# Kernel tuning notes

Hardware: AMD Instinct MI355X
Metric: run time of the kernel (lower is better)

Reference implementation:

```python
import jax, jax.numpy as jnp
import numpy as np

N = 100_000
E = 1_600_000
HID = 128
HEADS = 4
HD = HID // HEADS
EPS = 1e-5


def _ln(x, g, b):
    m = jnp.mean(x, axis=-1, keepdims=True)
    v = jnp.mean((x - m) ** 2, axis=-1, keepdims=True)
    return (x - m) * jax.lax.rsqrt(v + EPS) * g + b


def setup_inputs() -> dict:
    key = jax.random.key(0)
    ks = jax.random.split(key, 12)
    xav = lambda k, i, o: jax.random.uniform(k, (i, o), jnp.float32, -1.0, 1.0) * (0.1 * np.sqrt(6.0 / (i + o)))
    return {
        "h": jax.random.normal(ks[0], (N, HID), jnp.float32),
        "src": jax.random.randint(ks[1], (E,), 0, N, jnp.int32),
        "dst": jax.random.randint(ks[2], (E,), 0, N, jnp.int32),
        "Wq": xav(ks[3], HID, HID), "bq": jnp.zeros((HID,), jnp.float32),
        "Wk": xav(ks[4], HID, HID), "bk": jnp.zeros((HID,), jnp.float32),
        "Wv": xav(ks[5], HID, HID), "bv": jnp.zeros((HID,), jnp.float32),
        "Wo": xav(ks[6], HID, HID), "bo": jnp.zeros((HID,), jnp.float32),
        "W1": xav(ks[7], HID, 2 * HID), "b1": jnp.zeros((2 * HID,), jnp.float32),
        "W2": xav(ks[8], 2 * HID, HID), "b2": jnp.zeros((HID,), jnp.float32),
        "g1": jnp.ones((HID,), jnp.float32), "be1": jnp.zeros((HID,), jnp.float32),
        "g2": jnp.ones((HID,), jnp.float32), "be2": jnp.zeros((HID,), jnp.float32),
    }


def reference(h, src, dst, Wq, bq, Wk, bk, Wv, bv, Wo, bo, W1, b1, W2, b2, g1, be1, g2, be2):
    scale = HD ** -0.5
    h_norm = _ln(h, g1, be1)
    Q = (h_norm @ Wq + bq).reshape(N, HEADS, HD)
    K = (h_norm @ Wk + bk).reshape(N, HEADS, HD)
    V = (h_norm @ Wv + bv).reshape(N, HEADS, HD)

    # edge scores: q[dst] . k[src]  -> [E, HEADS]
    scores = jnp.sum(Q[dst] * K[src], axis=-1) * scale

    # edge softmax per destination node (segment softmax)
    smax = jax.ops.segment_max(scores, dst, num_segments=N)  # [N, HEADS]
    ex = jnp.exp(scores - smax[dst])
    denom = jax.ops.segment_sum(ex, dst, num_segments=N)
    alpha = ex / denom[dst]  # [E, HEADS]

    # weighted aggregation: sum over incoming edges of alpha * v[src]
    msgs = alpha[:, :, None] * V[src]  # [E, HEADS, HD]
    h_new = jax.ops.segment_sum(msgs, dst, num_segments=N).reshape(N, HID)

    h_attn = h_new @ Wo + bo
    h = h + h_attn  # dropout = identity (eval)
    h2 = _ln(h, g2, be2)
    ffn = jax.nn.relu(h2 @ W1 + b1) @ W2 + b2
    return h + ffn
```

## Files before the change

kernel.cpp:

```cpp
#include <hip/hip_runtime.h>
#include <math.h>

#define HIDN 128
#define EPS 1e-5f
#define ATT_SCALE 0.17677669529663687f

typedef unsigned int  u32;
typedef unsigned short u16;
typedef __attribute__((ext_vector_type(8))) short bf16x8;
typedef __attribute__((ext_vector_type(4))) float f32x4;

__device__ __forceinline__ u16 f2b(float x) {
    u32 u = __float_as_uint(x);
    u += 0x7FFFu + ((u >> 16) & 1u);
    return (u16)(u >> 16);
}
__device__ __forceinline__ float b2f(u16 x) { return __uint_as_float(((u32)x) << 16); }

#define MFMA(a, b, c) __builtin_amdgcn_mfma_f32_16x16x32_bf16((a), (b), (c), 0, 0, 0)

__device__ __forceinline__ int swz(int row, int kpos, int rowstride) {
    return row * rowstride + ((((kpos >> 3) ^ (row & 7)) << 3) | (kpos & 7));
}
__device__ __forceinline__ int swzf(int row, int kpos) {
    return row * 128 + ((((kpos >> 2) ^ (row & 7)) << 2) | (kpos & 3));
}

__global__ __launch_bounds__(256) void k_pack_all(
    const float* __restrict__ Wq, const float* __restrict__ Wk, const float* __restrict__ Wv,
    const float* __restrict__ Wo, const float* __restrict__ W1, const float* __restrict__ W2,
    u16* __restrict__ out)
{
    int idx = blockIdx.x * 256 + threadIdx.x;
    const float* W; int K, N, base, local;
    if      (idx <  2048) { W = Wq; K = 128; N = 128; base = 0;     local = idx; }
    else if (idx <  4096) { W = Wk; K = 128; N = 128; base = 16384; local = idx - 2048; }
    else if (idx <  6144) { W = Wv; K = 128; N = 128; base = 32768; local = idx - 4096; }
    else if (idx <  8192) { W = Wo; K = 128; N = 128; base = 49152; local = idx - 6144; }
    else if (idx < 12288) { W = W1; K = 128; N = 256; base = 65536; local = idx - 8192; }
    else if (idx < 16384) { W = W2; K = 256; N = 128; base = 98304; local = idx - 12288; }
    else return;
    const int KC = K >> 5;
    const int l  = local & 63;
    const int tc = local >> 6;
    const int c  = tc % KC;
    const int t  = tc / KC;
    const int col = l & 15, hg = l >> 4;
    const int kbase = c * 32 + hg * 8;
    u16 v[8];
    #pragma unroll
    for (int j = 0; j < 8; ++j) v[j] = f2b(W[(size_t)(kbase + j) * N + t * 16 + col]);
    uint4 o;
    o.x = (u32)v[0] | ((u32)v[1] << 16);
    o.y = (u32)v[2] | ((u32)v[3] << 16);
    o.z = (u32)v[4] | ((u32)v[5] << 16);
    o.w = (u32)v[6] | ((u32)v[7] << 16);
    *(uint4*)&out[base + local * 8] = o;
}

__global__ __launch_bounds__(256) void k_qkv(
    const float* __restrict__ h, const float* __restrict__ g1, const float* __restrict__ be1,
    const u16* __restrict__ Bq, const u16* __restrict__ Bk, const u16* __restrict__ Bv,
    const float* __restrict__ bq, const float* __restrict__ bk, const float* __restrict__ bv,
    u16* __restrict__ Q, u16* __restrict__ K, u16* __restrict__ V, int M)
{
    __shared__ u16 smem[4][2048];
    const int wid = threadIdx.x >> 6;
    const int l   = threadIdx.x & 63;
    int slab = blockIdx.x * 4 + wid;
    const bool valid = (slab * 16) < M;
    if (!valid) slab = 0;
    const int r0  = slab * 16;
    const int col = l & 15, hg = l >> 4;
    u16* ws = smem[wid];

    float av[4][8];
    const float* hr = h + (size_t)(r0 + col) * 128 + hg * 8;
    #pragma unroll
    for (int c = 0; c < 4; ++c) {
        float4 p0 = *(const float4*)&hr[c * 32];
        float4 p1 = *(const float4*)&hr[c * 32 + 4];
        av[c][0] = p0.x; av[c][1] = p0.y; av[c][2] = p0.z; av[c][3] = p0.w;
        av[c][4] = p1.x; av[c][5] = p1.y; av[c][6] = p1.z; av[c][7] = p1.w;
    }
    float s = 0.f, q2 = 0.f;
    #pragma unroll
    for (int c = 0; c < 4; ++c)
        #pragma unroll
        for (int j = 0; j < 8; ++j) { float v = av[c][j]; s += v; q2 += v * v; }
    s  += __shfl_xor(s, 16);  s  += __shfl_xor(s, 32);
    q2 += __shfl_xor(q2, 16); q2 += __shfl_xor(q2, 32);
    float mean = s * (1.f / 128.f);
    float var  = q2 * (1.f / 128.f) - mean * mean;
    float rs   = rsqrtf(var + EPS);

    bf16x8 af[4];
    #pragma unroll
    for (int c = 0; c < 4; ++c) {
        u32 w[4];
        #pragma unroll
        for (int jj = 0; jj < 4; ++jj) {
            int k0 = c * 32 + hg * 8 + 2 * jj;
            float v0 = (av[c][2 * jj]     - mean) * rs * g1[k0]     + be1[k0];
            float v1 = (av[c][2 * jj + 1] - mean) * rs * g1[k0 + 1] + be1[k0 + 1];
            w[jj] = (u32)f2b(v0) | ((u32)f2b(v1) << 16);
        }
        uint4 uu = make_uint4(w[0], w[1], w[2], w[3]);
        af[c] = *(bf16x8*)&uu;
    }

    const u16*  Bs[3] = {Bq, Bk, Bv};
    const float* bs[3] = {bq, bk, bv};
    u16*        Os[3] = {Q, K, V};
    #pragma unroll
    for (int w = 0; w < 3; ++w) {
        const u16* Bp = Bs[w];
        const float* bias = bs[w];
        #pragma unroll
        for (int t = 0; t < 8; ++t) {
            float bb = bias[t * 16 + col];
            f32x4 c = {bb, bb, bb, bb};
            const u16* bp = Bp + t * 2048 + l * 8;
            c = MFMA(af[0], *(const bf16x8*)(bp),        c);
            c = MFMA(af[1], *(const bf16x8*)(bp + 512),  c);
            c = MFMA(af[2], *(const bf16x8*)(bp + 1024), c);
            c = MFMA(af[3], *(const bf16x8*)(bp + 1536), c);
            #pragma unroll
            for (int r = 0; r < 4; ++r)
                ws[swz(hg * 4 + r, t * 16 + col, 128)] = f2b(c[r]);
        }
        __syncthreads();
        if (valid) {
            u16* O = Os[w];
            #pragma unroll
            for (int i = 0; i < 4; ++i) {
                int row = i * 4 + (l >> 4);
                int cg  = l & 15;
                bf16x8 vv = *(const bf16x8*)&ws[swz(row, cg * 8, 128)];
                *(bf16x8*)&O[(size_t)(r0 + row) * 128 + cg * 8] = vv;
            }
        }
        __syncthreads();
    }
}

#define BSH 8
#define CHUNK 4096

__global__ __launch_bounds__(256) void k_bcount(
    const int* __restrict__ dst, int* __restrict__ bcnt, int e)
{
    __shared__ int hist[512];
    const int tid = threadIdx.x;
    hist[tid] = 0; hist[tid + 256] = 0;
    __syncthreads();
    const int i0 = blockIdx.x * CHUNK;
    #pragma unroll
    for (int t = 0; t < CHUNK / 256; ++t) {
        int i = i0 + t * 256 + tid;
        if (i < e) atomicAdd(&hist[dst[i] >> BSH], 1);
    }
    __syncthreads();
    for (int j = tid; j < 512; j += 256) {
        int c = hist[j];
        if (c) atomicAdd(&bcnt[j], c);
    }
}

__global__ __launch_bounds__(512) void k_bscan(
    const int* __restrict__ bcnt, int* __restrict__ bbase, int* __restrict__ bcur, int nbuck)
{
    __shared__ int ts[512];
    const int tid = threadIdx.x;
    int v = (tid < nbuck) ? bcnt[tid] : 0;
    ts[tid] = v;
    __syncthreads();
    for (int off = 1; off < 512; off <<= 1) {
        int x = (tid >= off) ? ts[tid - off] : 0;
        __syncthreads();
        ts[tid] += x;
        __syncthreads();
    }
    int ex = ts[tid] - v;
    if (tid <= nbuck) bbase[tid] = ex;
    if (tid < nbuck)  bcur[tid]  = ex;
}

__global__ __launch_bounds__(256) void k_bscatter(
    const int* __restrict__ src, const int* __restrict__ dst,
    int* __restrict__ bcur, int2* __restrict__ ebuf, int e)
{
    __shared__ int hist[512];
    __shared__ int lbase[512];
    __shared__ int lrun[512];
    const int tid = threadIdx.x;
    hist[tid] = 0; hist[tid + 256] = 0;
    __syncthreads();
    const int i0 = blockIdx.x * CHUNK;
    #pragma unroll
    for (int t = 0; t < CHUNK / 256; ++t) {
        int i = i0 + t * 256 + tid;
        if (i < e) atomicAdd(&hist[dst[i] >> BSH], 1);
    }
    __syncthreads();
    for (int j = tid; j < 512; j += 256) {
        int c = hist[j];
        lrun[j] = 0;
        if (c) lbase[j] = atomicAdd(&bcur[j], c);
    }
    __syncthreads();
    #pragma unroll
    for (int t = 0; t < CHUNK / 256; ++t) {
        int i = i0 + t * 256 + tid;
        if (i < e) {
            int d = dst[i];
            int b = d >> BSH;
            int r = atomicAdd(&lrun[b], 1);
            ebuf[lbase[b] + r] = make_int2(src[i], d);
        }
    }
}

__global__ __launch_bounds__(256) void k_bbuild(
    const int2* __restrict__ ebuf, const int* __restrict__ bbase,
    int* __restrict__ cnt, int* __restrict__ offs, int* __restrict__ csrc, int n)
{
    __shared__ int ncnt[256];
    __shared__ int ts[256];
    __shared__ int nrun[256];
    const int tid = threadIdx.x;
    const int b = blockIdx.x;
    const int node0 = b << BSH;
    const int nn = min(256, n - node0);
    const int s = bbase[b];
    const int epb = bbase[b + 1] - s;

    ncnt[tid] = 0;
    __syncthreads();
    for (int i = tid; i < epb; i += 256)
        atomicAdd(&ncnt[ebuf[s + i].y & 255], 1);
    __syncthreads();
    int v = ncnt[tid];
    ts[tid] = v;
    __syncthreads();
    for (int off = 1; off < 256; off <<= 1) {
        int x = (tid >= off) ? ts[tid - off] : 0;
        __syncthreads();
        ts[tid] += x;
        __syncthreads();
    }
    int ex = ts[tid] - v;
    if (tid < nn) { cnt[node0 + tid] = v; offs[node0 + tid] = s + ex; }
    nrun[tid] = 0;
    __syncthreads();
    ncnt[tid] = ex;
    __syncthreads();
    for (int i = tid; i < epb; i += 256) {
        int2 p = ebuf[s + i];
        int d = p.y & 255;
        int r = atomicAdd(&nrun[d], 1);
        csrc[s + ncnt[d] + r] = p.x;
    }
}

__global__ __launch_bounds__(256) void k_edge(
    const u16* __restrict__ Qb, const u16* __restrict__ Kb, const u16* __restrict__ Vb,
    const int* __restrict__ offs, const int* __restrict__ cnt, const int* __restrict__ csrc,
    u16* __restrict__ hnew, int n)
{
    const int wid  = threadIdx.x >> 6;
    const int lane = threadIdx.x & 63;
    const int node = blockIdx.x * 4 + wid;
    if (node >= n) return;
    const int start = offs[node];
    const int deg   = cnt[node];

    const u32 qu = *(const u32*)&Qb[(size_t)node * 128 + lane * 2];
    const float q0 = b2f((u16)(qu & 0xFFFF));
    const float q1 = b2f((u16)(qu >> 16));

    float denom = 0.f, o0 = 0.f, o1 = 0.f;

    for (int base = 0; base < deg; base += 64) {
        int m = deg - base; if (m > 64) m = 64;
        int myidx = 0;
        if (lane < m) myidx = csrc[start + base + lane];
        int j = 0;
        for (; j + 4 <= m; j += 4) {
            int s0 = __shfl(myidx, j + 0);
            int s1 = __shfl(myidx, j + 1);
            int s2 = __shfl(myidx, j + 2);
            int s3 = __shfl(myidx, j + 3);
            const u32 k0 = *(const u32*)&Kb[(size_t)s0 * 128 + lane * 2];
            const u32 k1 = *(const u32*)&Kb[(size_t)s1 * 128 + lane * 2];
            const u32 k2 = *(const u32*)&Kb[(size_t)s2 * 128 + lane * 2];
            const u32 k3 = *(const u32*)&Kb[(size_t)s3 * 128 + lane * 2];
            const u32 v0 = *(const u32*)&Vb[(size_t)s0 * 128 + lane * 2];
            const u32 v1 = *(const u32*)&Vb[(size_t)s1 * 128 + lane * 2];
            const u32 v2 = *(const u32*)&Vb[(size_t)s2 * 128 + lane * 2];
            const u32 v3 = *(const u32*)&Vb[(size_t)s3 * 128 + lane * 2];
            float p0 = q0 * b2f((u16)(k0 & 0xFFFF)) + q1 * b2f((u16)(k0 >> 16));
            float p1 = q0 * b2f((u16)(k1 & 0xFFFF)) + q1 * b2f((u16)(k1 >> 16));
            float p2 = q0 * b2f((u16)(k2 & 0xFFFF)) + q1 * b2f((u16)(k2 >> 16));
            float p3 = q0 * b2f((u16)(k3 & 0xFFFF)) + q1 * b2f((u16)(k3 >> 16));
            p0 += __shfl_xor(p0, 1); p1 += __shfl_xor(p1, 1); p2 += __shfl_xor(p2, 1); p3 += __shfl_xor(p3, 1);
            p0 += __shfl_xor(p0, 2); p1 += __shfl_xor(p1, 2); p2 += __shfl_xor(p2, 2); p3 += __shfl_xor(p3, 2);
            p0 += __shfl_xor(p0, 4); p1 += __shfl_xor(p1, 4); p2 += __shfl_xor(p2, 4); p3 += __shfl_xor(p3, 4);
            p0 += __shfl_xor(p0, 8); p1 += __shfl_xor(p1, 8); p2 += __shfl_xor(p2, 8); p3 += __shfl_xor(p3, 8);
            float w0 = __expf(p0 * ATT_SCALE);
            float w1 = __expf(p1 * ATT_SCALE);
            float w2 = __expf(p2 * ATT_SCALE);
            float w3 = __expf(p3 * ATT_SCALE);
            denom += (w0 + w1) + (w2 + w3);
            o0 = fmaf(w0, b2f((u16)(v0 & 0xFFFF)), o0); o1 = fmaf(w0, b2f((u16)(v0 >> 16)), o1);
            o0 = fmaf(w1, b2f((u16)(v1 & 0xFFFF)), o0); o1 = fmaf(w1, b2f((u16)(v1 >> 16)), o1);
            o0 = fmaf(w2, b2f((u16)(v2 & 0xFFFF)), o0); o1 = fmaf(w2, b2f((u16)(v2 >> 16)), o1);
            o0 = fmaf(w3, b2f((u16)(v3 & 0xFFFF)), o0); o1 = fmaf(w3, b2f((u16)(v3 >> 16)), o1);
        }
        for (; j < m; ++j) {
            int s = __shfl(myidx, j);
            const u32 kk = *(const u32*)&Kb[(size_t)s * 128 + lane * 2];
            const u32 vv = *(const u32*)&Vb[(size_t)s * 128 + lane * 2];
            float p = q0 * b2f((u16)(kk & 0xFFFF)) + q1 * b2f((u16)(kk >> 16));
            p += __shfl_xor(p, 1); p += __shfl_xor(p, 2); p += __shfl_xor(p, 4); p += __shfl_xor(p, 8);
            float w = __expf(p * ATT_SCALE);
            denom += w;
            o0 = fmaf(w, b2f((u16)(vv & 0xFFFF)), o0);
            o1 = fmaf(w, b2f((u16)(vv >> 16)), o1);
        }
    }
    float inv = (deg > 0) ? (1.f / denom) : 0.f;
    u16 r0_ = f2b(o0 * inv), r1_ = f2b(o1 * inv);
    *(u32*)&hnew[(size_t)node * 128 + lane * 2] = (u32)r0_ | ((u32)r1_ << 16);
}

__global__ __launch_bounds__(256) void k_tail(
    const u16* __restrict__ hnew, const u16* __restrict__ Bo, const float* __restrict__ bo,
    const float* __restrict__ h, const float* __restrict__ g2, const float* __restrict__ be2,
    const u16* __restrict__ B1, const float* __restrict__ b1,
    const u16* __restrict__ B2, const float* __restrict__ b2,
    float* __restrict__ out, int M)
{
    __shared__ u16 smem[4][4096];
    const int wid = threadIdx.x >> 6;
    const int l   = threadIdx.x & 63;
    int slab = blockIdx.x * 4 + wid;
    const bool valid = (slab * 16) < M;
    if (!valid) slab = 0;
    const int r0  = slab * 16;
    const int col = l & 15, hg = l >> 4;
    u16* ws = smem[wid];

    const u16* ar = hnew + (size_t)(r0 + col) * 128 + hg * 8;
    bf16x8 a0 = *(const bf16x8*)(ar);
    bf16x8 a1 = *(const bf16x8*)(ar + 32);
    bf16x8 a2 = *(const bf16x8*)(ar + 64);
    bf16x8 a3 = *(const bf16x8*)(ar + 96);
    float h1v[8][4];
    float s[4] = {0, 0, 0, 0}, s2[4] = {0, 0, 0, 0};
    #pragma unroll
    for (int t = 0; t < 8; ++t) {
        float bb = bo[t * 16 + col];
        f32x4 c = {bb, bb, bb, bb};
        const u16* bp = Bo + t * 2048 + l * 8;
        c = MFMA(a0, *(const bf16x8*)(bp),        c);
        c = MFMA(a1, *(const bf16x8*)(bp + 512),  c);
        c = MFMA(a2, *(const bf16x8*)(bp + 1024), c);
        c = MFMA(a3, *(const bf16x8*)(bp + 1536), c);
        #pragma unroll
        for (int r = 0; r < 4; ++r) {
            float x = c[r] + h[(size_t)(r0 + hg * 4 + r) * 128 + t * 16 + col];
            h1v[t][r] = x;
            s[r] += x; s2[r] += x * x;
        }
    }
    float mean[4], rs[4];
    #pragma unroll
    for (int r = 0; r < 4; ++r) {
        float a = s[r], b = s2[r];
        a += __shfl_xor(a, 1); b += __shfl_xor(b, 1);
        a += __shfl_xor(a, 2); b += __shfl_xor(b, 2);
        a += __shfl_xor(a, 4); b += __shfl_xor(b, 4);
        a += __shfl_xor(a, 8); b += __shfl_xor(b, 8);
        mean[r] = a * (1.f / 128.f);
        float var = b * (1.f / 128.f) - mean[r] * mean[r];
        rs[r] = rsqrtf(var + EPS);
    }
    #pragma unroll
    for (int t = 0; t < 8; ++t) {
        float g  = g2[t * 16 + col];
        float be = be2[t * 16 + col];
        #pragma unroll
        for (int r = 0; r < 4; ++r)
            ws[swz(hg * 4 + r, t * 16 + col, 128)] =
                f2b((h1v[t][r] - mean[r]) * rs[r] * g + be);
    }
    __syncthreads();
    bf16x8 f1[4];
    #pragma unroll
    for (int i = 0; i < 4; ++i)
        f1[i] = *(const bf16x8*)&ws[swz(col, i * 32 + hg * 8, 128)];
    __syncthreads();
    #pragma unroll
    for (int t = 0; t < 16; ++t) {
        float bb = b1[t * 16 + col];
        f32x4 c = {bb, bb, bb, bb};
        const u16* bp = B1 + t * 2048 + l * 8;
        c = MFMA(f1[0], *(const bf16x8*)(bp),        c);
        c = MFMA(f1[1], *(const bf16x8*)(bp + 512),  c);
        c = MFMA(f1[2], *(const bf16x8*)(bp + 1024), c);
        c = MFMA(f1[3], *(const bf16x8*)(bp + 1536), c);
        #pragma unroll
        for (int r = 0; r < 4; ++r)
            ws[swz(hg * 4 + r, t * 16 + col, 256)] = f2b(fmaxf(c[r], 0.f));
    }
    __syncthreads();
    bf16x8 f2[8];
    #pragma unroll
    for (int i = 0; i < 8; ++i)
        f2[i] = *(const bf16x8*)&ws[swz(col, i * 32 + hg * 8, 256)];
    __syncthreads();
    float* wsf = (float*)ws;
    #pragma unroll
    for (int t = 0; t < 8; ++t) {
        float bb = b2[t * 16 + col];
        f32x4 c = {bb, bb, bb, bb};
        const u16* bp = B2 + t * 4096 + l * 8;
        #pragma unroll
        for (int kc = 0; kc < 8; ++kc)
            c = MFMA(f2[kc], *(const bf16x8*)(bp + kc * 512), c);
        #pragma unroll
        for (int r = 0; r < 4; ++r)
            wsf[swzf(hg * 4 + r, t * 16 + col)] = c[r] + h1v[t][r];
    }
    __syncthreads();
    if (valid) {
        #pragma unroll
        for (int i = 0; i < 8; ++i) {
            int row = i * 2 + (l >> 5);
            int cg  = l & 31;
            float4 v = *(const float4*)&wsf[swzf(row, cg * 4)];
            *(float4*)&out[(size_t)(r0 + row) * 128 + cg * 4] = v;
        }
    }
}

extern "C" void kernel_launch(void* const* d_in, const int* in_sizes, int n_in,
                              void* d_out, int out_size, void* d_ws, size_t ws_size,
                              hipStream_t stream)
{
    const float* h   = (const float*)d_in[0];
    const int*   src = (const int*)  d_in[1];
    const int*   dst = (const int*)  d_in[2];
    const float* Wq  = (const float*)d_in[3];
    const float* bq  = (const float*)d_in[4];
    const float* Wk  = (const float*)d_in[5];
    const float* bk  = (const float*)d_in[6];
    const float* Wv  = (const float*)d_in[7];
    const float* bv  = (const float*)d_in[8];
    const float* Wo  = (const float*)d_in[9];
    const float* bo  = (const float*)d_in[10];
    const float* W1  = (const float*)d_in[11];
    const float* b1  = (const float*)d_in[12];
    const float* W2  = (const float*)d_in[13];
    const float* b2  = (const float*)d_in[14];
    const float* g1  = (const float*)d_in[15];
    const float* be1 = (const float*)d_in[16];
    const float* g2  = (const float*)d_in[17];
    const float* be2 = (const float*)d_in[18];

    const int n = in_sizes[0] / HIDN;
    const int e = in_sizes[1];
    float* out = (float*)d_out;

    const int nbuck = (n + 255) >> BSH;

    char* p = (char*)d_ws;
    int* csrc  = (int*)p;              p += (size_t)e * 4;
    int* cnt   = (int*)p;              p += (size_t)n * 4;
    int* offs  = (int*)p;              p += (size_t)n * 4;
    int* bcnt  = (int*)p;              p += 512 * 4;
    int* bbase = (int*)p;              p += 512 * 4;
    int* bcur  = (int*)p;              p += 512 * 4;
    u16* wpack = (u16*)p;              p += 131072 * 2;
    const size_t NB = (size_t)n * HIDN * 2;
    u16* Qb   = (u16*)p;               p += NB;
    u16* Kb   = (u16*)p;               p += NB;
    u16* Vb   = (u16*)p;               p += NB;
    u16* hnew = (u16*)p;               p += NB;
    int2* ebuf = (int2*)p;             p += (size_t)e * 8;

    u16* Wq_p = wpack;
    u16* Wk_p = wpack + 16384;
    u16* Wv_p = wpack + 32768;
    u16* Wo_p = wpack + 49152;
    u16* W1_p = wpack + 65536;
    u16* W2_p = wpack + 98304;

    const int nslab = (n + 15) / 16;
    const int gemm_blocks = (nslab + 3) / 4;
    const int echunks = (e + CHUNK - 1) / CHUNK;

    hipMemsetAsync(bcnt, 0, 512 * sizeof(int), stream);

    k_bcount  <<<echunks, 256, 0, stream>>>(dst, bcnt, e);
    k_bscan   <<<1, 512, 0, stream>>>(bcnt, bbase, bcur, nbuck);
    k_bscatter<<<echunks, 256, 0, stream>>>(src, dst, bcur, ebuf, e);
    k_bbuild  <<<nbuck, 256, 0, stream>>>(ebuf, bbase, cnt, offs, csrc, n);

    k_pack_all<<<64, 256, 0, stream>>>(Wq, Wk, Wv, Wo, W1, W2, wpack);

    k_qkv <<<gemm_blocks, 256, 0, stream>>>(h, g1, be1, Wq_p, Wk_p, Wv_p,
                                            bq, bk, bv, Qb, Kb, Vb, n);

    k_edge<<<(n + 3) / 4, 256, 0, stream>>>(Qb, Kb, Vb, offs, cnt, csrc, hnew, n);

    k_tail<<<gemm_blocks, 256, 0, stream>>>(hnew, Wo_p, bo, h, g2, be2,
                                            W1_p, b1, W2_p, b2, out, n);
}
```

Before: 485.4 us.

## Interleave K/V in fp16, use dot2 edge kernel, split tail into three kernels

```diff
diff --git a/kernel.cpp b/kernel.cpp
--- a/kernel.cpp
+++ b/kernel.cpp
@@ -9,6 +9,7 @@
 typedef unsigned short u16;
 typedef __attribute__((ext_vector_type(8))) short bf16x8;
 typedef __attribute__((ext_vector_type(4))) float f32x4;
+typedef __attribute__((ext_vector_type(2))) _Float16 h16x2;
 
 __device__ __forceinline__ u16 f2b(float x) {
     u32 u = __float_as_uint(x);
@@ -16,14 +17,25 @@
     return (u16)(u >> 16);
 }
 __device__ __forceinline__ float b2f(u16 x) { return __uint_as_float(((u32)x) << 16); }
+__device__ __forceinline__ u16 f2h(float x) {
+    _Float16 h = (_Float16)x;
+    u16 r; __builtin_memcpy(&r, &h, 2); return r;
+}
+__device__ __forceinline__ h16x2 u2h(u32 a) { h16x2 r; __builtin_memcpy(&r, &a, 4); return r; }
+
+__device__ __forceinline__ float dot2f(u32 a, u32 b, float c) {
+    h16x2 ah = u2h(a), bh = u2h(b);
+#if __has_builtin(__builtin_amdgcn_fdot2)
+    return __builtin_amdgcn_fdot2(ah, bh, c, false);
+#else
+    return c + (float)ah.x * (float)bh.x + (float)ah.y * (float)bh.y;
+#endif
+}
 
 #define MFMA(a, b, c) __builtin_amdgcn_mfma_f32_16x16x32_bf16((a), (b), (c), 0, 0, 0)
 
 __device__ __forceinline__ int swz(int row, int kpos, int rowstride) {
     return row * rowstride + ((((kpos >> 3) ^ (row & 7)) << 3) | (kpos & 7));
-}
-__device__ __forceinline__ int swzf(int row, int kpos) {
-    return row * 128 + ((((kpos >> 2) ^ (row & 7)) << 2) | (kpos & 3));
 }
 
 __global__ __launch_bounds__(256) void k_pack_all(
@@ -62,9 +74,9 @@
     const float* __restrict__ h, const float* __restrict__ g1, const float* __restrict__ be1,
     const u16* __restrict__ Bq, const u16* __restrict__ Bk, const u16* __restrict__ Bv,
     const float* __restrict__ bq, const float* __restrict__ bk, const float* __restrict__ bv,
-    u16* __restrict__ Q, u16* __restrict__ K, u16* __restrict__ V, int M)
-{
-    __shared__ u16 smem[4][2048];
+    u16* __restrict__ Qh, u16* __restrict__ KVb, int M)
+{
+    __shared__ u16 smem[4][4096];
     const int wid = threadIdx.x >> 6;
     const int l   = threadIdx.x & 63;
     int slab = blockIdx.x * 4 + wid;
@@ -109,38 +121,70 @@
         af[c] = *(bf16x8*)&uu;
     }
 
-    const u16*  Bs[3] = {Bq, Bk, Bv};
-    const float* bs[3] = {bq, bk, bv};
-    u16*        Os[3] = {Q, K, V};
-    #pragma unroll
-    for (int w = 0; w < 3; ++w) {
-        const u16* Bp = Bs[w];
-        const float* bias = bs[w];
-        #pragma unroll
-        for (int t = 0; t < 8; ++t) {
-            float bb = bias[t * 16 + col];
-            f32x4 c = {bb, bb, bb, bb};
-            const u16* bp = Bp + t * 2048 + l * 8;
-            c = MFMA(af[0], *(const bf16x8*)(bp),        c);
-            c = MFMA(af[1], *(const bf16x8*)(bp + 512),  c);
-            c = MFMA(af[2], *(const bf16x8*)(bp + 1024), c);
-            c = MFMA(af[3], *(const bf16x8*)(bp + 1536), c);
-            #pragma unroll
-            for (int r = 0; r < 4; ++r)
-                ws[swz(hg * 4 + r, t * 16 + col, 128)] = f2b(c[r]);
-        }
-        __syncthreads();
-        if (valid) {
-            u16* O = Os[w];
-            #pragma unroll
-            for (int i = 0; i < 4; ++i) {
-                int row = i * 4 + (l >> 4);
-                int cg  = l & 15;
-                bf16x8 vv = *(const bf16x8*)&ws[swz(row, cg * 8, 128)];
-                *(bf16x8*)&O[(size_t)(r0 + row) * 128 + cg * 8] = vv;
-            }
-        }
-        __syncthreads();
+    #pragma unroll
+    for (int t = 0; t < 8; ++t) {
+        float bb = bq[t * 16 + col];
+        f32x4 c = {bb, bb, bb, bb};
+        const u16* bp = Bq + t * 2048 + l * 8;
+        c = MFMA(af[0], *(const bf16x8*)(bp),        c);
+        c = MFMA(af[1], *(const bf16x8*)(bp + 512),  c);
+        c = MFMA(af[2], *(const bf16x8*)(bp + 1024), c);
+        c = MFMA(af[3], *(const bf16x8*)(bp + 1536), c);
+        #pragma unroll
+        for (int r = 0; r < 4; ++r)
+            ws[swz(hg * 4 + r, t * 16 + col, 256)] = f2h(c[r]);
+    }
+    __syncthreads();
+    if (valid) {
+        #pragma unroll
+        for (int i = 0; i < 4; ++i) {
+            int row = i * 4 + (l >> 4);
+            int cg  = l & 15;
+            bf16x8 vv = *(const bf16x8*)&ws[swz(row, cg * 8, 256)];
+            *(bf16x8*)&Qh[(size_t)(r0 + row) * 128 + cg * 8] = vv;
+        }
+    }
+    __syncthreads();
+
+    #pragma unroll
+    for (int t = 0; t < 8; ++t) {
+        float bb = bk[t * 16 + col];
+        f32x4 c = {bb, bb, bb, bb};
+        const u16* bp = Bk + t * 2048 + l * 8;
+        c = MFMA(af[0], *(const bf16x8*)(bp),        c);
+        c = MFMA(af[1], *(const bf16x8*)(bp + 512),  c);
+        c = MFMA(af[2], *(const bf16x8*)(bp + 1024), c);
+        c = MFMA(af[3], *(const bf16x8*)(bp + 1536), c);
+        int cc = t * 16 + col;
+        int kp = ((cc >> 1) << 2) | (cc & 1);
+        #pragma unroll
+        for (int r = 0; r < 4; ++r)
+            ws[swz(hg * 4 + r, kp, 256)] = f2h(c[r]);
+    }
+    #pragma unroll
+    for (int t = 0; t < 8; ++t) {
+        float bb = bv[t * 16 + col];
+        f32x4 c = {bb, bb, bb, bb};
+        const u16* bp = Bv + t * 2048 + l * 8;
+        c = MFMA(af[0], *(const bf16x8*)(bp),        c);
+        c = MFMA(af[1], *(const bf16x8*)(bp + 512),  c);
+        c = MFMA(af[2], *(const bf16x8*)(bp + 1024), c);
+        c = MFMA(af[3], *(const bf16x8*)(bp + 1536), c);
+        int cc = t * 16 + col;
+        int kp = ((cc >> 1) << 2) | 2 | (cc & 1);
+        #pragma unroll
+        for (int r = 0; r < 4; ++r)
+            ws[swz(hg * 4 + r, kp, 256)] = f2h(c[r]);
+    }
+    __syncthreads();
+    if (valid) {
+        #pragma unroll
+        for (int i = 0; i < 8; ++i) {
+            int row = i * 2 + (l >> 5);
+            int g   = l & 31;
+            bf16x8 vv = *(const bf16x8*)&ws[swz(row, g * 8, 256)];
+            *(bf16x8*)&KVb[(size_t)(r0 + row) * 256 + g * 8] = vv;
+        }
     }
 }
 
@@ -264,100 +308,87 @@
 }
 
 __global__ __launch_bounds__(256) void k_edge(
-    const u16* __restrict__ Qb, const u16* __restrict__ Kb, const u16* __restrict__ Vb,
+    const u16* __restrict__ Qh, const u16* __restrict__ KVb,
     const int* __restrict__ offs, const int* __restrict__ cnt, const int* __restrict__ csrc,
     u16* __restrict__ hnew, int n)
 {
     const int wid  = threadIdx.x >> 6;
-    const int lane = threadIdx.x & 63;
+    const int l    = threadIdx.x & 63;
     const int node = blockIdx.x * 4 + wid;
     if (node >= n) return;
     const int start = offs[node];
     const int deg   = cnt[node];
-
-    const u32 qu = *(const u32*)&Qb[(size_t)node * 128 + lane * 2];
-    const float q0 = b2f((u16)(qu & 0xFFFF));
-    const float q1 = b2f((u16)(qu >> 16));
-
-    float denom = 0.f, o0 = 0.f, o1 = 0.f;
+    const int w    = l & 15;
+    const int slot = l >> 4;
+
+    const uint4 q = *(const uint4*)&Qh[(size_t)node * 128 + w * 8];
+
+    h16x2 o0 = {0, 0}, o1 = {0, 0}, o2 = {0, 0}, o3 = {0, 0};
+    float denom = 0.f;
 
     for (int base = 0; base < deg; base += 64) {
         int m = deg - base; if (m > 64) m = 64;
         int myidx = 0;
-        if (lane < m) myidx = csrc[start + base + lane];
-        int j = 0;
-        for (; j + 4 <= m; j += 4) {
-            int s0 = __shfl(myidx, j + 0);
-            int s1 = __shfl(myidx, j + 1);
-            int s2 = __shfl(myidx, j + 2);
-            int s3 = __shfl(myidx, j + 3);
-            const u32 k0 = *(const u32*)&Kb[(size_t)s0 * 128 + lane * 2];
-            const u32 k1 = *(const u32*)&Kb[(size_t)s1 * 128 + lane * 2];
-            const u32 k2 = *(const u32*)&Kb[(size_t)s2 * 128 + lane * 2];
-            const u32 k3 = *(const u32*)&Kb[(size_t)s3 * 128 + lane * 2];
-            const u32 v0 = *(const u32*)&Vb[(size_t)s0 * 128 + lane * 2];
-            const u32 v1 = *(const u32*)&Vb[(size_t)s1 * 128 + lane * 2];
-            const u32 v2 = *(const u32*)&Vb[(size_t)s2 * 128 + lane * 2];
-            const u32 v3 = *(const u32*)&Vb[(size_t)s3 * 128 + lane * 2];
-            float p0 = q0 * b2f((u16)(k0 & 0xFFFF)) + q1 * b2f((u16)(k0 >> 16));
-            float p1 = q0 * b2f((u16)(k1 & 0xFFFF)) + q1 * b2f((u16)(k1 >> 16));
-            float p2 = q0 * b2f((u16)(k2 & 0xFFFF)) + q1 * b2f((u16)(k2 >> 16));
-            float p3 = q0 * b2f((u16)(k3 & 0xFFFF)) + q1 * b2f((u16)(k3 >> 16));
-            p0 += __shfl_xor(p0, 1); p1 += __shfl_xor(p1, 1); p2 += __shfl_xor(p2, 1); p3 += __shfl_xor(p3, 1);
-            p0 += __shfl_xor(p0, 2); p1 += __shfl_xor(p1, 2); p2 += __shfl_xor(p2, 2); p3 += __shfl_xor(p3, 2);
-            p0 += __shfl_xor(p0, 4); p1 += __shfl_xor(p1, 4); p2 += __shfl_xor(p2, 4); p3 += __shfl_xor(p3, 4);
-            p0 += __shfl_xor(p0, 8); p1 += __shfl_xor(p1, 8); p2 += __shfl_xor(p2, 8); p3 += __shfl_xor(p3, 8);
-            float w0 = __expf(p0 * ATT_SCALE);
-            float w1 = __expf(p1 * ATT_SCALE);
-            float w2 = __expf(p2 * ATT_SCALE);
-            float w3 = __expf(p3 * ATT_SCALE);
-            denom += (w0 + w1) + (w2 + w3);
-            o0 = fmaf(w0, b2f((u16)(v0 & 0xFFFF)), o0); o1 = fmaf(w0, b2f((u16)(v0 >> 16)), o1);
-            o0 = fmaf(w1, b2f((u16)(v1 & 0xFFFF)), o0); o1 = fmaf(w1, b2f((u16)(v1 >> 16)), o1);
-            o0 = fmaf(w2, b2f((u16)(v2 & 0xFFFF)), o0); o1 = fmaf(w2, b2f((u16)(v2 >> 16)), o1);
-            o0 = fmaf(w3, b2f((u16)(v3 & 0xFFFF)), o0); o1 = fmaf(w3, b2f((u16)(v3 >> 16)), o1);
-        }
-        for (; j < m; ++j) {
-            int s = __shfl(myidx, j);
-            const u32 kk = *(const u32*)&Kb[(size_t)s * 128 + lane * 2];
-            const u32 vv = *(const u32*)&Vb[(size_t)s * 128 + lane * 2];
-            float p = q0 * b2f((u16)(kk & 0xFFFF)) + q1 * b2f((u16)(kk >> 16));
-            p += __shfl_xor(p, 1); p += __shfl_xor(p, 2); p += __shfl_xor(p, 4); p += __shfl_xor(p, 8);
-            float w = __expf(p * ATT_SCALE);
-            denom += w;
-            o0 = fmaf(w, b2f((u16)(vv & 0xFFFF)), o0);
-            o1 = fmaf(w, b2f((u16)(vv >> 16)), o1);
-        }
+        if (l < m) myidx = csrc[start + base + l];
+        for (int j = 0; j < m; j += 4) {
+            int eloc = j + slot;
+            int s = __shfl(myidx, eloc & 63);
+            const u16* kvr = KVb + (size_t)s * 256 + w * 16;
+            uint4 kv0 = *(const uint4*)(kvr);
+            uint4 kv1 = *(const uint4*)(kvr + 8);
+            float p = dot2f(kv0.x, q.x, 0.f);
+            p = dot2f(kv0.z, q.y, p);
+            p = dot2f(kv1.x, q.z, p);
+            p = dot2f(kv1.z, q.w, p);
+            p += __shfl_xor(p, 1);
+            p += __shfl_xor(p, 2);
+            float al = __expf(p * ATT_SCALE);
+            al = (eloc < m) ? al : 0.f;
+            denom += al;
+            h16x2 a2; a2.x = (_Float16)al; a2.y = a2.x;
+            o0 += a2 * u2h(kv0.y);
+            o1 += a2 * u2h(kv0.w);
+            o2 += a2 * u2h(kv1.y);
+            o3 += a2 * u2h(kv1.w);
+        }
+    }
+
+    float of[8];
+    of[0] = (float)o0.x; of[1] = (float)o0.y; of[2] = (float)o1.x; of[3] = (float)o1.y;
+    of[4] = (float)o2.x; of[5] = (float)o2.y; of[6] = (float)o3.x; of[7] = (float)o3.y;
+    #pragma unroll
+    for (int msk = 16; msk <= 32; msk <<= 1) {
+        #pragma unroll
+        for (int i = 0; i < 8; ++i) of[i] += __shfl_xor(of[i], msk);
+        denom += __shfl_xor(denom, msk);
     }
     float inv = (deg > 0) ? (1.f / denom) : 0.f;
-    u16 r0_ = f2b(o0 * inv), r1_ = f2b(o1 * inv);
-    *(u32*)&hnew[(size_t)node * 128 + lane * 2] = (u32)r0_ | ((u32)r1_ << 16);
-}
-
-__global__ __launch_bounds__(256) void k_tail(
+    if (slot == 0) {
+        u32 wrd[4];
+        #pragma unroll
+        for (int i = 0; i < 4; ++i)
+            wrd[i] = (u32)f2b(of[2 * i] * inv) | ((u32)f2b(of[2 * i + 1] * inv) << 16);
+        uint4 uu = make_uint4(wrd[0], wrd[1], wrd[2], wrd[3]);
+        *(uint4*)&hnew[(size_t)node * 128 + w * 8] = uu;
+    }
+}
+
+__global__ __launch_bounds__(256) void k_attnout(
     const u16* __restrict__ hnew, const u16* __restrict__ Bo, const float* __restrict__ bo,
     const float* __restrict__ h, const float* __restrict__ g2, const float* __restrict__ be2,
-    const u16* __restrict__ B1, const float* __restrict__ b1,
-    const u16* __restrict__ B2, const float* __restrict__ b2,
-    float* __restrict__ out, int M)
-{
-    __shared__ u16 smem[4][4096];
-    const int wid = threadIdx.x >> 6;
-    const int l   = threadIdx.x & 63;
-    int slab = blockIdx.x * 4 + wid;
-    const bool valid = (slab * 16) < M;
-    if (!valid) slab = 0;
-    const int r0  = slab * 16;
+    float* __restrict__ h1, u16* __restrict__ h2, int M)
+{
+    const int slab = blockIdx.x * 4 + (threadIdx.x >> 6);
+    const int l = threadIdx.x & 63;
+    const int r0 = slab * 16;
+    if (r0 >= M) return;
     const int col = l & 15, hg = l >> 4;
-    u16* ws = smem[wid];
-
     const u16* ar = hnew + (size_t)(r0 + col) * 128 + hg * 8;
     bf16x8 a0 = *(const bf16x8*)(ar);
     bf16x8 a1 = *(const bf16x8*)(ar + 32);
     bf16x8 a2 = *(const bf16x8*)(ar + 64);
     bf16x8 a3 = *(const bf16x8*)(ar + 96);
-    float h1v[8][4];
-    float s[4] = {0, 0, 0, 0}, s2[4] = {0, 0, 0, 0};
+    f32x4 acc[8];
     #pragma unroll
     for (int t = 0; t < 8; ++t) {
         float bb = bo[t * 16 + col];
@@ -367,10 +398,15 @@
         c = MFMA(a1, *(const bf16x8*)(bp + 512),  c);
         c = MFMA(a2, *(const bf16x8*)(bp + 1024), c);
         c = MFMA(a3, *(const bf16x8*)(bp + 1536), c);
+        acc[t] = c;
+    }
+    float s[4] = {0, 0, 0, 0}, s2[4] = {0, 0, 0, 0};
+    #pragma unroll
+    for (int t = 0; t < 8; ++t) {
         #pragma unroll
         for (int r = 0; r < 4; ++r) {
-            float x = c[r] + h[(size_t)(r0 + hg * 4 + r) * 128 + t * 16 + col];
-            h1v[t][r] = x;
+            float x = acc[t][r] + h[(size_t)(r0 + hg * 4 + r) * 128 + t * 16 + col];
+            acc[t][r] = x;
             s[r] += x; s2[r] += x * x;
         }
     }
@@ -391,36 +427,57 @@
         float g  = g2[t * 16 + col];
         float be = be2[t * 16 + col];
         #pragma unroll
-        for (int r = 0; r < 4; ++r)
-            ws[swz(hg * 4 + r, t * 16 + col, 128)] =
-                f2b((h1v[t][r] - mean[r]) * rs[r] * g + be);
-    }
-    __syncthreads();
-    bf16x8 f1[4];
-    #pragma unroll
-    for (int i = 0; i < 4; ++i)
-        f1[i] = *(const bf16x8*)&ws[swz(col, i * 32 + hg * 8, 128)];
-    __syncthreads();
+        for (int r = 0; r < 4; ++r) {
+            size_t idx = (size_t)(r0 + hg * 4 + r) * 128 + t * 16 + col;
+            float x = acc[t][r];
+            h1[idx] = x;
+            h2[idx] = f2b((x - mean[r]) * rs[r] * g + be);
+        }
+    }
+}
+
+__global__ __launch_bounds__(256) void k_ffn1(
+    const u16* __restrict__ h2, const u16* __restrict__ B1, const float* __restrict__ b1,
+    u16* __restrict__ tb, int M)
+{
+    const int slab = blockIdx.x * 4 + (threadIdx.x >> 6);
+    const int l = threadIdx.x & 63;
+    const int r0 = slab * 16;
+    if (r0 >= M) return;
+    const int col = l & 15, hg = l >> 4;
+    const u16* ar = h2 + (size_t)(r0 + col) * 128 + hg * 8;
+    bf16x8 a0 = *(const bf16x8*)(ar);
+    bf16x8 a1 = *(const bf16x8*)(ar + 32);
+    bf16x8 a2 = *(const bf16x8*)(ar + 64);
+    bf16x8 a3 = *(const bf16x8*)(ar + 96);
     #pragma unroll
     for (int t = 0; t < 16; ++t) {
         float bb = b1[t * 16 + col];
         f32x4 c = {bb, bb, bb, bb};
         const u16* bp = B1 + t * 2048 + l * 8;
-        c = MFMA(f1[0], *(const bf16x8*)(bp),        c);
-        c = MFMA(f1[1], *(const bf16x8*)(bp + 512),  c);
-        c = MFMA(f1[2], *(const bf16x8*)(bp + 1024), c);
-        c = MFMA(f1[3], *(const bf16x8*)(bp + 1536), c);
+        c = MFMA(a0, *(const bf16x8*)(bp),        c);
+        c = MFMA(a1, *(const bf16x8*)(bp + 512),  c);
+        c = MFMA(a2, *(const bf16x8*)(bp + 1024), c);
+        c = MFMA(a3, *(const bf16x8*)(bp + 1536), c);
         #pragma unroll
         for (int r = 0; r < 4; ++r)
-            ws[swz(hg * 4 + r, t * 16 + col, 256)] = f2b(fmaxf(c[r], 0.f));
-    }
-    __syncthreads();
-    bf16x8 f2[8];
-    #pragma unroll
-    for (int i = 0; i < 8; ++i)
-        f2[i] = *(const bf16x8*)&ws[swz(col, i * 32 + hg * 8, 256)];
-    __syncthreads();
-    float* wsf = (float*)ws;
+            tb[(size_t)(r0 + hg * 4 + r) * 256 + t * 16 + col] = f2b(fmaxf(c[r], 0.f));
+    }
+}
+
+__global__ __launch_bounds__(256) void k_ffn2(
+    const u16* __restrict__ tb, const u16* __restrict__ B2, const float* __restrict__ b2,
+    const float* __restrict__ h1, float* __restrict__ out, int M)
+{
+    const int slab = blockIdx.x * 4 + (threadIdx.x >> 6);
+    const int l = threadIdx.x & 63;
+    const int r0 = slab * 16;
+    if (r0 >= M) return;
+    const int col = l & 15, hg = l >> 4;
+    const u16* ar = tb + (size_t)(r0 + col) * 256 + hg * 8;
+    bf16x8 a[8];
+    #pragma unroll
+    for (int i = 0; i < 8; ++i) a[i] = *(const bf16x8*)(ar + i * 32);
     #pragma unroll
     for (int t = 0; t < 8; ++t) {
         float bb = b2[t * 16 + col];
@@ -428,19 +485,11 @@
         const u16* bp = B2 + t * 4096 + l * 8;
         #pragma unroll
         for (int kc = 0; kc < 8; ++kc)
-            c = MFMA(f2[kc], *(const bf16x8*)(bp + kc * 512), c);
-        #pragma unroll
-        for (int r = 0; r < 4; ++r)
-            wsf[swzf(hg * 4 + r, t * 16 + col)] = c[r] + h1v[t][r];
-    }
-    __syncthreads();
-    if (valid) {
-        #pragma unroll
-        for (int i = 0; i < 8; ++i) {
-            int row = i * 2 + (l >> 5);
-            int cg  = l & 31;
-            float4 v = *(const float4*)&wsf[swzf(row, cg * 4)];
-            *(float4*)&out[(size_t)(r0 + row) * 128 + cg * 4] = v;
+            c = MFMA(a[kc], *(const bf16x8*)(bp + kc * 512), c);
+        #pragma unroll
+        for (int r = 0; r < 4; ++r) {
+            size_t idx = (size_t)(r0 + hg * 4 + r) * 128 + t * 16 + col;
+            out[idx] = c[r] + h1[idx];
         }
     }
 }
@@ -483,12 +532,13 @@
     int* bbase = (int*)p;              p += 512 * 4;
     int* bcur  = (int*)p;              p += 512 * 4;
     u16* wpack = (u16*)p;              p += 131072 * 2;
-    const size_t NB = (size_t)n * HIDN * 2;
-    u16* Qb   = (u16*)p;               p += NB;
-    u16* Kb   = (u16*)p;               p += NB;
-    u16* Vb   = (u16*)p;               p += NB;
-    u16* hnew = (u16*)p;               p += NB;
-    int2* ebuf = (int2*)p;             p += (size_t)e * 8;
+    u16* KVb  = (u16*)p;               p += (size_t)n * 256 * 2;
+    u16* Qh   = (u16*)p;               p += (size_t)n * 128 * 2;
+    u16* hnew = (u16*)p;               p += (size_t)n * 128 * 2;
+    float* h1 = (float*)p;             p += (size_t)n * 128 * 4;
+    u16* h2 = Qh;
+    u16* tb = KVb;
+    int2* ebuf = (int2*)h1;
 
     u16* Wq_p = wpack;
     u16* Wk_p = wpack + 16384;
@@ -511,10 +561,13 @@
     k_pack_all<<<64, 256, 0, stream>>>(Wq, Wk, Wv, Wo, W1, W2, wpack);
 
     k_qkv <<<gemm_blocks, 256, 0, stream>>>(h, g1, be1, Wq_p, Wk_p, Wv_p,
-                                            bq, bk, bv, Qb, Kb, Vb, n);
-
-    k_edge<<<(n + 3) / 4, 256, 0, stream>>>(Qb, Kb, Vb, offs, cnt, csrc, hnew, n);
-
-    k_tail<<<gemm_blocks, 256, 0, stream>>>(hnew, Wo_p, bo, h, g2, be2,
-                                            W1_p, b1, W2_p, b2, out, n);
-}
+                                            bq, bk, bv, Qh, KVb, n);
+
+    k_edge<<<(n + 3) / 4, 256, 0, stream>>>(Qh, KVb, offs, cnt, csrc, hnew, n);
+
+    k_attnout<<<gemm_blocks, 256, 0, stream>>>(hnew, Wo_p, bo, h, g2, be2, h1, h2, n);
+
+    k_ffn1<<<gemm_blocks, 256, 0, stream>>>(h2, W1_p, b1, tb, n);
+
+    k_ffn2<<<gemm_blocks, 256, 0, stream>>>(tb, W2_p, b2, h1, out, n);
+}
```

After: 464.6 us. 4.3% less time.
